# Kernel optimization log

Measured on AMD Instinct MI355X. Metric: run time of the kernel, lower is better.

Reference implementation:

```python
import jax, jax.numpy as jnp
import numpy as np

B, S, D, H, FD = 2, 2048, 1024, 16, 64
DK = D // H
ALPHA = 1.0


def _l2norm(t):
    # matches F.normalize(p=2, dim=-1): divide by max(norm, eps)
    n = jnp.linalg.norm(t, axis=-1, keepdims=True)
    return t / jnp.maximum(n, 1e-12)


def setup_inputs() -> dict:
    key = jax.random.key(0)
    ks = jax.random.split(key, 12)
    sc = 0.02
    return {
        "x": jax.random.normal(ks[0], (B, S, D), jnp.float32),
        "features": jax.random.normal(ks[1], (B, S, FD), jnp.float32),
        "requirements": jax.random.normal(ks[2], (B, S, FD), jnp.float32),
        "Wq": jax.random.normal(ks[3], (D, D), jnp.float32) * sc,
        "bq": jnp.zeros((D,), jnp.float32),
        "Wk": jax.random.normal(ks[4], (D, D), jnp.float32) * sc,
        "bk": jnp.zeros((D,), jnp.float32),
        "Wv": jax.random.normal(ks[5], (D, D), jnp.float32) * sc,
        "bv": jnp.zeros((D,), jnp.float32),
        "Wo": jax.random.normal(ks[6], (D, D), jnp.float32) * sc,
        "bo": jnp.zeros((D,), jnp.float32),
        "pos_ids": jax.random.randint(ks[7], (B, S), 0, 8),
        "causal_mask": jnp.tril(jnp.ones((S, S), bool)),
    }


def reference(x, features, requirements, Wq, bq, Wk, bk, Wv, bv, Wo, bo,
              pos_ids, causal_mask):
    # q/k/v projections -> [B, S, H, DK]
    Q = (x @ Wq + bq).reshape(B, S, H, DK)
    K = (x @ Wk + bk).reshape(B, S, H, DK)
    V = (x @ Wv + bv).reshape(B, S, H, DK)

    # scaled QK^T: [B, H, S, S]
    scores = jnp.einsum('bshd,bthd->bhst', Q, K) / np.sqrt(DK).astype(np.float32)

    # ASA bias (features_only mode): cosine compat req_i . feat_j -> [B, S, S]
    bias = jnp.einsum('bsf,btf->bst', _l2norm(requirements), _l2norm(features))
    scores = scores + ALPHA * bias[:, None, :, :]

    # causal mask (True = allowed)
    scores = jnp.where(causal_mask[None, None, :, :], scores, -jnp.inf)

    weights = jax.nn.softmax(scores, axis=-1)
    weights = jnp.nan_to_num(weights, nan=0.0)

    out = jnp.einsum('bhst,bthd->bshd', weights, V).reshape(B, S, D)
    return out @ Wo + bo
```

## Files before the change

### kernel.cpp

```cpp
#include <hip/hip_runtime.h>
#include <hip/hip_bf16.h>
#include <math.h>

#define Bb 2
#define Ss 2048
#define Dd 1024
#define Hh 16
#define DK 64
#define FD 64

#define LOG2E 1.4426950408889634f

typedef short short8 __attribute__((ext_vector_type(8)));
typedef float f32x4 __attribute__((ext_vector_type(4)));
typedef unsigned int u32;

static __device__ inline ushort f2bf(float f) {
    union { float f; unsigned u; } v; v.f = f;
    unsigned r = v.u + 0x7FFF + ((v.u >> 16) & 1);
    return (ushort)(r >> 16);
}

static __device__ inline uint cvt_pk_bf16(float lo, float hi) {
    uint r;
    asm("v_cvt_pk_bf16_f32 %0, %1, %2" : "=v"(r) : "v"(lo), "v"(hi));
    return r;
}
static __device__ inline float fexp2(float x) {
    return __builtin_amdgcn_exp2f(x);
}

static __device__ inline void gload_lds16(const ushort* g, ushort* l) {
    __builtin_amdgcn_global_load_lds((const __attribute__((address_space(1))) u32*)g,
                                     (__attribute__((address_space(3))) u32*)l, 16, 0, 0);
}

__global__ __launch_bounds__(256) void prep(const float* __restrict__ x,
                                            const float* __restrict__ features,
                                            const float* __restrict__ requirements,
                                            const float* __restrict__ W0,
                                            const float* __restrict__ W1,
                                            const float* __restrict__ W2,
                                            const float* __restrict__ W3,
                                            ushort* __restrict__ WT,
                                            ushort* __restrict__ xb,
                                            ushort* __restrict__ Qext,
                                            ushort* __restrict__ Kext) {
    __shared__ float T[64][65];
    const int blk = blockIdx.x;
    const int tid = threadIdx.x;

    if (blk < 8192) {
        size_t p = (size_t)blk * 256 + tid;
        float2 v = *(const float2*)(x + 2 * p);
        ((uint*)xb)[p] = (uint)f2bf(v.x) | ((uint)f2bf(v.y) << 16);
        return;
    }
    if (blk < 9216) {
        const int f = blk - 8192;
        const int bx = f & 15, by = (f >> 4) & 15, bz = f >> 8;
        const float* W = bz == 0 ? W0 : bz == 1 ? W1 : bz == 2 ? W2 : W3;
        ushort* dst = WT + (size_t)bz * Dd * Dd;
        const int k0 = bx * 64, n0 = by * 64;
#pragma unroll
        for (int i = 0; i < 4; ++i) {
            int kr = i * 16 + (tid >> 4);
            int nc = (tid & 15) * 4;
            float4 v = *(const float4*)(W + (size_t)(k0 + kr) * Dd + n0 + nc);
            T[kr][nc] = v.x; T[kr][nc + 1] = v.y; T[kr][nc + 2] = v.z; T[kr][nc + 3] = v.w;
        }
        __syncthreads();
        int nr = tid >> 2;
        int kc = (tid & 3) * 16;
        uint pk[8];
#pragma unroll
        for (int j = 0; j < 8; ++j)
            pk[j] = (uint)f2bf(T[kc + 2 * j][nr]) | ((uint)f2bf(T[kc + 2 * j + 1][nr]) << 16);
        uint* o = (uint*)(dst + (size_t)(n0 + nr) * Dd + k0 + kc);
        *(int4*)o = *(int4*)&pk[0];
        *(int4*)(o + 4) = *(int4*)&pk[4];
        return;
    }
    {
        const int f3 = blk - 9216;
        const int row = f3 * 4 + (tid >> 6);
        const int lane = tid & 63;
        const int b = row >> 11, s = row & (Ss - 1);
        const int j = lane & 31;
        const float* src = (lane < 32) ? features : requirements;
        float2 v = *(const float2*)(src + (size_t)row * FD + 2 * j);
        float ss = v.x * v.x + v.y * v.y;
#pragma unroll
        for (int off = 16; off; off >>= 1) ss += __shfl_xor(ss, off, 64);
        const float inv = 1.0f / fmaxf(sqrtf(ss), 1e-12f);
        const float scl = (lane < 32) ? inv : inv * LOG2E;
        const uint pk = cvt_pk_bf16(v.x * scl, v.y * scl);
        uint* dstq = (uint*)Qext;
        uint* dstk = (uint*)Kext;
#pragma unroll
        for (int h = 0; h < 16; ++h) {
            size_t rowq = ((size_t)(b * Hh + h) * Ss + s) * 64 + 32 + j;
            if (lane < 32) dstk[rowq] = pk;
            else           dstq[rowq] = pk;
        }
    }
}

__global__ __launch_bounds__(256) void pack_vt(const ushort* __restrict__ Vrow,
                                               ushort* __restrict__ Vt) {
    __shared__ ushort T[64][72];
    const int tid = threadIdx.x;
    const int s0 = blockIdx.x * 64;
    const int h = blockIdx.y, b = blockIdx.z;
#pragma unroll
    for (int i = 0; i < 2; ++i) {
        int f = tid + i * 256;
        int sr = f >> 3, dc = (f & 7) * 8;
        *(int4*)&T[sr][dc] =
            *(const int4*)(Vrow + ((size_t)((b * Hh + h) * Ss) + s0 + sr) * 64 + dc);
    }
    __syncthreads();
    int d = tid >> 2;
    int sg = (tid & 3) * 16;
    uint pk[8];
#pragma unroll
    for (int j = 0; j < 8; ++j)
        pk[j] = (uint)T[sg + 2 * j][d] | ((uint)T[sg + 2 * j + 1][d] << 16);
    uint* dst = (uint*)(Vt + ((size_t)((b * Hh + h) * DK + d)) * Ss + s0 + sg);
    *(int4*)dst = *(int4*)&pk[0];
    *(int4*)(dst + 4) = *(int4*)&pk[4];
}

__global__ __launch_bounds__(256) void gemm_qkv(const ushort* __restrict__ xb,
                                                const ushort* __restrict__ WT,
                                                const float* __restrict__ bq,
                                                const float* __restrict__ bk,
                                                const float* __restrict__ bv,
                                                ushort* __restrict__ Qext,
                                                ushort* __restrict__ Kext,
                                                ushort* __restrict__ Vrow) {
    __shared__ ushort smem[17408];
    ushort (*As)[64] = (ushort (*)[64])smem;
    ushort (*Bs)[64] = (ushort (*)[64])(smem + 8192);
    const int tid = threadIdx.x;
    const int lane = tid & 63, wave = tid >> 6;
    const int col = lane & 15, quad = lane >> 4;
    const int wm = wave >> 1, wn = wave & 1;
    const int flat = blockIdx.x + 24 * blockIdx.y;
    const int xcd = flat & 7;
    const int jj = flat >> 3;
    const int id = jj % 3;
    const int n0 = xcd * 128;
    const int m0 = (jj / 3) * 128;
    const ushort* BTw = WT + (size_t)id * Dd * Dd;
    const float* bias = id == 0 ? bq : id == 1 ? bk : bv;

    const int l8 = lane >> 3;
    const int srcg = (lane & 7) ^ l8;
    const ushort* aS[4]; const ushort* bS[4];
    ushort* aD[4]; ushort* bD[4];
#pragma unroll
    for (int i = 0; i < 4; ++i) {
        int r = wave * 32 + i * 8 + l8;
        aS[i] = xb  + (size_t)(m0 + r) * Dd + srcg * 8;
        bS[i] = BTw + (size_t)(n0 + r) * Dd + srcg * 8;
        aD[i] = smem + (wave * 4 + i) * 512;
        bD[i] = smem + 8192 + (wave * 4 + i) * 512;
    }
    const int xs = col & 7;

    f32x4 acc[4][4] = {};

    for (int k0 = 0; k0 < Dd; k0 += 64) {
        __syncthreads();
#pragma unroll
        for (int i = 0; i < 4; ++i) {
            gload_lds16(aS[i] + k0, aD[i]);
            gload_lds16(bS[i] + k0, bD[i]);
        }
        __syncthreads();
#pragma unroll
        for (int kk = 0; kk < 2; ++kk) {
            short8 af[4], bf[4];
#pragma unroll
            for (int i = 0; i < 4; ++i) {
                af[i] = *(const short8*)&As[wm * 64 + i * 16 + col][((kk * 4 + quad) ^ xs) * 8];
                bf[i] = *(const short8*)&Bs[wn * 64 + i * 16 + col][((kk * 4 + quad) ^ xs) * 8];
            }
#pragma unroll
            for (int i = 0; i < 4; ++i)
#pragma unroll
                for (int j = 0; j < 4; ++j)
                    acc[i][j] = __builtin_amdgcn_mfma_f32_16x16x32_bf16(af[i], bf[j], acc[i][j], 0, 0, 0);
        }
    }

    __syncthreads();
    ushort (*Ep)[136] = (ushort (*)[136])smem;
    const float scl = (id == 0) ? 0.125f * LOG2E : 1.0f;
#pragma unroll
    for (int j = 0; j < 4; ++j) {
        int n_local = wn * 64 + j * 16 + col;
        float bvl = bias[n0 + n_local];
#pragma unroll
        for (int i = 0; i < 4; ++i) {
            int mb = wm * 64 + i * 16 + quad * 4;
#pragma unroll
            for (int reg = 0; reg < 4; ++reg)
                Ep[mb + reg][n_local] = f2bf((acc[i][j][reg] + bvl) * scl);
        }
    }
    __syncthreads();
    {
        const int mrow = tid >> 1;
        const int half = tid & 1;
        const int b = m0 >> 11, s = (m0 & (Ss - 1)) + mrow;
        const int hh = (n0 >> 6) + half;
        if (id == 2) {
            ushort* drow = Vrow + ((size_t)(b * Hh + hh) * Ss + s) * 64;
#pragma unroll
            for (int k = 0; k < 8; ++k)
                *(int4*)(drow + k * 8) = *(int4*)&Ep[mrow][half * 64 + k * 8];
        } else {
            ushort* drow = (id == 0 ? Qext : Kext) + ((size_t)(b * Hh + hh) * Ss + s) * 128;
#pragma unroll
            for (int k = 0; k < 8; ++k)
                *(int4*)(drow + k * 8) = *(int4*)&Ep[mrow][half * 64 + k * 8];
        }
    }
}

__global__ __launch_bounds__(256) void gemm_out(const ushort* __restrict__ Ab,
                                                const ushort* __restrict__ BT,
                                                const float* __restrict__ bias,
                                                float* __restrict__ C) {
    __shared__ ushort As[128][64];
    __shared__ ushort Bs[128][64];
    const int tid = threadIdx.x;
    const int lane = tid & 63, wave = tid >> 6;
    const int col = lane & 15, quad = lane >> 4;
    const int wm = wave >> 1, wn = wave & 1;
    const int n0 = blockIdx.x * 128;
    const int m0 = blockIdx.y * 128;

    const int l8 = lane >> 3;
    const int srcg = (lane & 7) ^ l8;
    const ushort* aS[4]; const ushort* bS[4];
    ushort* aD[4]; ushort* bD[4];
#pragma unroll
    for (int i = 0; i < 4; ++i) {
        int r = wave * 32 + i * 8 + l8;
        aS[i] = Ab + (size_t)(m0 + r) * Dd + srcg * 8;
        bS[i] = BT + (size_t)(n0 + r) * Dd + srcg * 8;
        aD[i] = &As[0][0] + (wave * 4 + i) * 512;
        bD[i] = &Bs[0][0] + (wave * 4 + i) * 512;
    }
    const int xs = col & 7;

    f32x4 acc[4][4] = {};

    for (int k0 = 0; k0 < Dd; k0 += 64) {
        __syncthreads();
#pragma unroll
        for (int i = 0; i < 4; ++i) {
            gload_lds16(aS[i] + k0, aD[i]);
            gload_lds16(bS[i] + k0, bD[i]);
        }
        __syncthreads();
#pragma unroll
        for (int kk = 0; kk < 2; ++kk) {
            short8 af[4], bf[4];
#pragma unroll
            for (int i = 0; i < 4; ++i) {
                af[i] = *(const short8*)&As[wm * 64 + i * 16 + col][((kk * 4 + quad) ^ xs) * 8];
                bf[i] = *(const short8*)&Bs[wn * 64 + i * 16 + col][((kk * 4 + quad) ^ xs) * 8];
            }
#pragma unroll
            for (int i = 0; i < 4; ++i)
#pragma unroll
                for (int j = 0; j < 4; ++j)
                    acc[i][j] = __builtin_amdgcn_mfma_f32_16x16x32_bf16(af[i], bf[j], acc[i][j], 0, 0, 0);
        }
    }

#pragma unroll
    for (int j = 0; j < 4; ++j) {
        int n = n0 + wn * 64 + j * 16 + col;
        float bvl = bias[n];
#pragma unroll
        for (int i = 0; i < 4; ++i) {
#pragma unroll
            for (int reg = 0; reg < 4; ++reg) {
                int m = m0 + wm * 64 + i * 16 + quad * 4 + reg;
                C[(size_t)m * Dd + n] = acc[i][j][reg] + bvl;
            }
        }
    }
}

__global__ __launch_bounds__(256) void attn_mfma15(const ushort* __restrict__ Qe,
                                                   const ushort* __restrict__ Ke,
                                                   const ushort* __restrict__ Vt,
                                                   ushort* __restrict__ Ob) {
    __shared__ ushort Ks[64][128];
    __shared__ ushort Vts[64][64];
    __shared__ ushort PsT[4][16][64];

    const int tid = threadIdx.x;
    const int wave = tid >> 6, lane = tid & 63;
    const int col = lane & 15, quad = lane >> 4;

    const int id = blockIdx.x;
    const int x = id & 7;
    const int j = id >> 3;
    const int half = j & 1;
    const int bhi = ((j >> 6) & 1) * 2 + ((j >> 1) & 1);
    const int qh = (j >> 2) & 7;
    const int rep = (j >> 5) & 1;
    const int bh = bhi * 8 + x;
    const int qt = rep ? (15 - qh) : qh;
    const int b = bh >> 4, h = bh & 15;
    const int q0 = qt * 128 + half * 64;
    const int rowb = q0 + wave * 16;

    short8 qf[4];
    {
        const ushort* qp = Qe + ((size_t)bh * Ss + rowb + col) * 128 + quad * 8;
#pragma unroll
        for (int k0 = 0; k0 < 4; ++k0) qf[k0] = *(const short8*)(qp + k0 * 32);
    }

    const f32x4 zero4 = {0.f, 0.f, 0.f, 0.f};
    f32x4 oaccT[4] = {zero4, zero4, zero4, zero4};
    float lsum = 0.f;

    const ushort* Kbase = Ke + (size_t)bh * Ss * 128;
    const ushort* Vbase = Vt + (size_t)bh * 64 * Ss;
    const int xsw = col & 7;

    const ushort* kS[4]; ushort* kD[4];
#pragma unroll
    for (int i = 0; i < 4; ++i) {
        int G = i * 256 + tid;
        int r = G >> 4, g = G & 15;
        kS[i] = Kbase + (size_t)r * 128 + (g ^ (r & 7)) * 8;
        kD[i] = &Ks[0][0] + (i * 256 + wave * 64) * 8;
    }
    const ushort* vS[2]; ushort* vD[2];
#pragma unroll
    for (int i = 0; i < 2; ++i) {
        int G = i * 256 + tid;
        int r = G >> 3, g = G & 7;
        vS[i] = Vbase + (size_t)r * Ss + (g ^ (r & 7)) * 8;
        vD[i] = &Vts[0][0] + (i * 256 + wave * 64) * 8;
    }

    const int ntiles = 2 * qt + half + 1;
    for (int t = 0; t < ntiles; ++t) {
        const int j0 = t * 64;
        const size_t ko = (size_t)j0 * 128;
        __syncthreads();
#pragma unroll
        for (int i = 0; i < 4; ++i) gload_lds16(kS[i] + ko, kD[i]);
#pragma unroll
        for (int i = 0; i < 2; ++i) gload_lds16(vS[i] + j0, vD[i]);
        __syncthreads();

        if (j0 > rowb + 15) continue;

        f32x4 sacc[4] = {zero4, zero4, zero4, zero4};
        __builtin_amdgcn_s_setprio(1);
#pragma unroll
        for (int c = 0; c < 4; ++c)
#pragma unroll
            for (int k0 = 0; k0 < 4; ++k0) {
                short8 kf = *(const short8*)&Ks[c * 16 + col][((k0 * 4 + quad) ^ xsw) * 8];
                sacc[c] = __builtin_amdgcn_mfma_f32_16x16x32_bf16(kf, qf[k0], sacc[c], 0, 0, 0);
            }
        __builtin_amdgcn_s_setprio(0);

        const bool diag = (j0 + 63 >= rowb);
        if (diag) {
            const int qrow_rel = rowb + col - j0;
#pragma unroll
            for (int c = 0; c < 4; ++c)
#pragma unroll
                for (int reg = 0; reg < 4; ++reg) {
                    float s = sacc[c][reg];
                    if (c * 16 + quad * 4 + reg > qrow_rel) s = -1e9f;
                    float p = fexp2(fminf(s, 28.853901f));
                    lsum += p;
                    sacc[c][reg] = p;
                }
        } else {
#pragma unroll
            for (int c = 0; c < 4; ++c)
#pragma unroll
                for (int reg = 0; reg < 4; ++reg) {
                    float p = fexp2(fminf(sacc[c][reg], 28.853901f));
                    lsum += p;
                    sacc[c][reg] = p;
                }
        }
#pragma unroll
        for (int c = 0; c < 4; ++c) {
            uint2 pk;
            pk.x = cvt_pk_bf16(sacc[c][0], sacc[c][1]);
            pk.y = cvt_pk_bf16(sacc[c][2], sacc[c][3]);
            *(uint2*)&PsT[wave][col][((c * 2 + (quad >> 1)) ^ xsw) * 8 + (quad & 1) * 4] = pk;
        }

        __builtin_amdgcn_s_setprio(1);
#pragma unroll
        for (int k0 = 0; k0 < 2; ++k0) {
            short8 ptf = *(const short8*)&PsT[wave][col][((k0 * 4 + quad) ^ xsw) * 8];
#pragma unroll
            for (int c2 = 0; c2 < 4; ++c2) {
                short8 vtf = *(const short8*)&Vts[c2 * 16 + col][((k0 * 4 + quad) ^ xsw) * 8];
                oaccT[c2] = __builtin_amdgcn_mfma_f32_16x16x32_bf16(vtf, ptf, oaccT[c2], 0, 0, 0);
            }
        }
        __builtin_amdgcn_s_setprio(0);
    }

    {
        float l = lsum;
        l += __shfl_xor(l, 16, 64);
        l += __shfl_xor(l, 32, 64);
        const float inv = 1.f / l;
        ushort* dst = Ob + ((size_t)b * Ss + rowb + col) * Dd + h * DK + quad * 4;
#pragma unroll
        for (int c2 = 0; c2 < 4; ++c2) {
            uint2 pk;
            pk.x = cvt_pk_bf16(oaccT[c2][0] * inv, oaccT[c2][1] * inv);
            pk.y = cvt_pk_bf16(oaccT[c2][2] * inv, oaccT[c2][3] * inv);
            *(uint2*)(dst + c2 * 16) = pk;
        }
    }
}

extern "C" void kernel_launch(void* const* d_in, const int* in_sizes, int n_in,
                              void* d_out, int out_size, void* d_ws, size_t ws_size,
                              hipStream_t stream) {
    const float* x            = (const float*)d_in[0];
    const float* features     = (const float*)d_in[1];
    const float* requirements = (const float*)d_in[2];
    const float* Wq = (const float*)d_in[3];
    const float* bq = (const float*)d_in[4];
    const float* Wk = (const float*)d_in[5];
    const float* bk = (const float*)d_in[6];
    const float* Wv = (const float*)d_in[7];
    const float* bv = (const float*)d_in[8];
    const float* Wo = (const float*)d_in[9];
    const float* bo = (const float*)d_in[10];

    float* out = (float*)d_out;
    float* ws = (float*)d_ws;

    ushort* xb   = (ushort*)(ws);
    ushort* WT   = (ushort*)(ws + 2097152);
    ushort* Qext = (ushort*)(ws + 4194304);
    ushort* Kext = (ushort*)(ws + 8388608);
    ushort* Vrow = (ushort*)(ws + 12582912);
    ushort* Vt   = (ushort*)(ws + 16777216);
    ushort* abb  = (ushort*)(ws + 12582912);

    prep<<<10240, 256, 0, stream>>>(x, features, requirements, Wq, Wk, Wv, Wo,
                                    WT, xb, Qext, Kext);

    gemm_qkv<<<dim3(24, 32), 256, 0, stream>>>(xb, WT, bq, bk, bv, Qext, Kext, Vrow);
    pack_vt<<<dim3(Ss / 64, Hh, Bb), 256, 0, stream>>>(Vrow, Vt);

    attn_mfma15<<<dim3(1024), 256, 0, stream>>>(Qext, Kext, Vt, abb);

    gemm_out<<<dim3(8, 32), 256, 0, stream>>>(abb, WT + (size_t)3 * Dd * Dd, bo, out);
}
```

Baseline: 240.1 us.

## Use 128-row query tiles with 8-wave attention blocks sharing K/V loads

The attention kernel now processes 128 query rows per block with 512 threads (8 waves) instead of 64 rows with 4 waves, so each K/V tile loaded into LDS feeds twice as many query rows. This halves the number of blocks and the redundant global K/V traffic. Block-to-tile mapping is rewritten to pair light and heavy causal tiles for load balance, and the per-thread load addressing is simplified to incrementing pointers. The tradeoff is fewer blocks for latency hiding and more waves idling at diagonal tiles.

```diff
diff --git a/kernel.cpp b/kernel.cpp
--- a/kernel.cpp
+++ b/kernel.cpp
@@ -298,13 +298,15 @@
     }
 }
 
-__global__ __launch_bounds__(256) void attn_mfma15(const ushort* __restrict__ Qe,
+#define ABQ 128
+
+__global__ __launch_bounds__(512) void attn_mfma14(const ushort* __restrict__ Qe,
                                                    const ushort* __restrict__ Ke,
                                                    const ushort* __restrict__ Vt,
                                                    ushort* __restrict__ Ob) {
     __shared__ ushort Ks[64][128];
     __shared__ ushort Vts[64][64];
-    __shared__ ushort PsT[4][16][64];
+    __shared__ ushort PsT[8][16][64];
 
     const int tid = threadIdx.x;
     const int wave = tid >> 6, lane = tid & 63;
@@ -312,15 +314,15 @@
 
     const int id = blockIdx.x;
     const int x = id & 7;
-    const int j = id >> 3;
-    const int half = j & 1;
-    const int bhi = ((j >> 6) & 1) * 2 + ((j >> 1) & 1);
-    const int qh = (j >> 2) & 7;
-    const int rep = (j >> 5) & 1;
+    const int k = id >> 3;
+    const int rep = k & 1;
+    const int bhi = (k >> 1) & 3;
+    const int qh = k >> 3;
     const int bh = bhi * 8 + x;
-    const int qt = rep ? (15 - qh) : qh;
+    const int qt = rep ? (qh < 4 ? qh + 4 : 15 - qh)
+                       : (qh < 4 ? qh : 19 - qh);
     const int b = bh >> 4, h = bh & 15;
-    const int q0 = qt * 128 + half * 64;
+    const int q0 = qt * ABQ;
     const int rowb = q0 + wave * 16;
 
     short8 qf[4];
@@ -338,32 +340,26 @@
     const ushort* Vbase = Vt + (size_t)bh * 64 * Ss;
     const int xsw = col & 7;
 
-    const ushort* kS[4]; ushort* kD[4];
-#pragma unroll
-    for (int i = 0; i < 4; ++i) {
-        int G = i * 256 + tid;
-        int r = G >> 4, g = G & 15;
-        kS[i] = Kbase + (size_t)r * 128 + (g ^ (r & 7)) * 8;
-        kD[i] = &Ks[0][0] + (i * 256 + wave * 64) * 8;
-    }
-    const ushort* vS[2]; ushort* vD[2];
-#pragma unroll
-    for (int i = 0; i < 2; ++i) {
-        int G = i * 256 + tid;
-        int r = G >> 3, g = G & 7;
-        vS[i] = Vbase + (size_t)r * Ss + (g ^ (r & 7)) * 8;
-        vD[i] = &Vts[0][0] + (i * 256 + wave * 64) * 8;
-    }
-
-    const int ntiles = 2 * qt + half + 1;
+    const int Gk0 = wave * 64 + lane;
+    const int rk0 = Gk0 >> 4, sk0 = (Gk0 & 15) ^ (rk0 & 7);
+    const int Gk1 = 512 + Gk0;
+    const int rk1 = Gk1 >> 4, sk1 = (Gk1 & 15) ^ (rk1 & 7);
+    const int Gv = Gk0;
+    const int rv = Gv >> 3, sv = (Gv & 7) ^ (rv & 7);
+    const ushort* ksrc0 = Kbase + (size_t)rk0 * 128 + sk0 * 8;
+    const ushort* ksrc1 = Kbase + (size_t)rk1 * 128 + sk1 * 8;
+    const ushort* vsrc  = Vbase + (size_t)rv * Ss + sv * 8;
+    ushort* kdst0 = &Ks[0][0] + wave * 512;
+    ushort* kdst1 = &Ks[0][0] + 4096 + wave * 512;
+    ushort* vdst  = &Vts[0][0] + wave * 512;
+
+    const int ntiles = 2 * qt + 2;
     for (int t = 0; t < ntiles; ++t) {
         const int j0 = t * 64;
-        const size_t ko = (size_t)j0 * 128;
-        __syncthreads();
-#pragma unroll
-        for (int i = 0; i < 4; ++i) gload_lds16(kS[i] + ko, kD[i]);
-#pragma unroll
-        for (int i = 0; i < 2; ++i) gload_lds16(vS[i] + j0, vD[i]);
+        __syncthreads();
+        gload_lds16(ksrc0, kdst0);   ksrc0 += 64 * 128;
+        gload_lds16(ksrc1, kdst1);   ksrc1 += 64 * 128;
+        gload_lds16(vsrc,  vdst);    vsrc  += 64;
         __syncthreads();
 
         if (j0 > rowb + 15) continue;
@@ -471,7 +467,7 @@
     gemm_qkv<<<dim3(24, 32), 256, 0, stream>>>(xb, WT, bq, bk, bv, Qext, Kext, Vrow);
     pack_vt<<<dim3(Ss / 64, Hh, Bb), 256, 0, stream>>>(Vrow, Vt);
 
-    attn_mfma15<<<dim3(1024), 256, 0, stream>>>(Qext, Kext, Vt, abb);
+    attn_mfma14<<<dim3(512), 512, 0, stream>>>(Qext, Kext, Vt, abb);
 
     gemm_out<<<dim3(8, 32), 256, 0, stream>>>(abb, WT + (size_t)3 * Dd * Dd, bo, out);
 }
```

Result: faster. 234.0 us (-2.6%).
